# Performance work log

Hardware: AMD Instinct MI355X
Metric: run time of the kernel (lower is better)

Reference implementation:

```python
import jax, jax.numpy as jnp
import numpy as np

N = 20000      # atom nodes
E_UND = 200000 # undirected edges -> E = 2*E_UND directed, stored as interleaved reverse pairs
D = 128        # hid_dim
H = 4          # heads (fixed in MVMP)
DEPTH = 3


def _build_graph():
    rng = np.random.default_rng(0)
    u_chain = np.arange(N - 1)
    v_chain = u_chain + 1
    n_extra = E_UND - (N - 1)
    ue = rng.integers(0, N, n_extra)
    ve = rng.integers(0, N, n_extra)
    ve = np.where(ue == ve, (ve + 1) % N, ve)
    u = np.concatenate([u_chain, ue])
    v = np.concatenate([v_chain, ve])
    # interleave so that edge 2k = u->v and edge 2k+1 = v->u (reverse_edge pairing)
    src = np.stack([u, v], 1).reshape(-1).astype(np.int32)
    dst = np.stack([v, u], 1).reshape(-1).astype(np.int32)
    return jnp.asarray(src), jnp.asarray(dst)


def setup_inputs() -> dict:
    key = jax.random.key(0)
    ks = jax.random.split(key, 10)
    src, dst = _build_graph()
    E = src.shape[0]
    s = 1.0 / np.sqrt(D)

    def lin(k, shape):
        return (jax.random.normal(k, shape, jnp.float32) * s).astype(jnp.float32)

    return {
        "f": jax.random.normal(ks[0], (N, D), jnp.float32),
        "x": jax.random.normal(ks[1], (E, D), jnp.float32),
        "src": src,
        "dst": dst,
        "Wq": lin(ks[2], (D, D)), "bq": jnp.zeros((D,), jnp.float32),
        "Wk": lin(ks[3], (D, D)), "bk": jnp.zeros((D,), jnp.float32),
        "Wv": lin(ks[4], (D, D)), "bv": jnp.zeros((D,), jnp.float32),
        "Wo": lin(ks[5], (D, D)), "bo": jnp.zeros((D,), jnp.float32),
        "W_mp": lin(ks[6], (DEPTH - 1, D, D)),
        "b_mp": jnp.zeros((DEPTH - 1, D), jnp.float32),
        "W_last": lin(ks[7], (3 * D, D)),
        "b_last": jnp.zeros((D,), jnp.float32),
    }


def _mailbox_attention(f_h, h, dst, Wq, bq, Wk, bk, Wv, bv, Wo, bo):
    """add_attn: per-node MHA with query = node state, keys/values = incoming edge msgs.
    Implemented as an edge-segment softmax (no padding), equivalent to DGL degree bucketing."""
    n = f_h.shape[0]
    dk = D // H
    q = (f_h @ Wq + bq).reshape(n, H, dk)     # [N,H,dk]
    k = (h @ Wk + bk).reshape(-1, H, dk)      # [E,H,dk]
    v = (h @ Wv + bv).reshape(-1, H, dk)      # [E,H,dk]
    scores = jnp.einsum("ehd,ehd->eh", q[dst], k) / jnp.sqrt(jnp.float32(dk))  # [E,H]
    smax = jax.ops.segment_max(scores, dst, num_segments=n)   # [N,H]
    p = jnp.exp(scores - smax[dst])
    denom = jax.ops.segment_sum(p, dst, num_segments=n)       # [N,H]
    ctx = jax.ops.segment_sum(p[:, :, None] * v, dst, num_segments=n) / denom[:, :, None]
    out = ctx.reshape(n, D) @ Wo + bo
    return out + f_h  # residual in add_attn


def reference(f, x, src, dst, Wq, bq, Wk, bk, Wv, bv, Wo, bo, W_mp, b_mp, W_last, b_last):
    n, E = f.shape[0], x.shape[0]
    f_h = f          # init_node: f_h = f.clone()
    h = x            # init_edge: h = x.clone()
    for i in range(DEPTH - 1):
        # multi_update_all: copy_e('h','m') then add_attn on node states
        f_h = _mailbox_attention(f_h, h, dst, Wq, bq, Wk, bk, Wv, bv, Wo, bo)
        # rev_h = reverse_edge(h): swap interleaved pairs
        rev_h = h.reshape(E // 2, 2, D)[:, ::-1, :].reshape(E, D)
        # del_reverse_message: m = f_h[src] - rev_h
        m = f_h[src] - rev_h
        # update_edge: h = relu(x + Linear_i(m))
        h = jax.nn.relu(x + m @ W_mp[i] + b_mp[i])
    # final: copy_e('h','mail') then update_node with Linear(3D->D)
    mail = jax.ops.segment_sum(h, dst, num_segments=n)
    return jnp.concatenate([mail, f_h, f], axis=1) @ W_last + b_last
```

## Files before the change

### kernel.cpp

```cpp
#include <hip/hip_runtime.h>
#include <hip/hip_bf16.h>

typedef __attribute__((ext_vector_type(8))) short bf16x8;
typedef __attribute__((ext_vector_type(4))) float f32x4;

__device__ __forceinline__ unsigned short f2bf(float f) {
    unsigned u = __float_as_uint(f);
    unsigned r = (u + 0x7FFFu + ((u >> 16) & 1u)) >> 16;
    return (unsigned short)r;
}
__device__ __forceinline__ float bf2f(unsigned short b) {
    return __uint_as_float(((unsigned)b) << 16);
}
__device__ __forceinline__ unsigned pack2(float a, float b) {
    return (unsigned)f2bf(a) | ((unsigned)f2bf(b) << 16);
}
__device__ __forceinline__ unsigned pksub(unsigned a, unsigned b) {
    float r0 = bf2f((unsigned short)(a & 0xffff)) - bf2f((unsigned short)(b & 0xffff));
    float r1 = bf2f((unsigned short)(a >> 16))    - bf2f((unsigned short)(b >> 16));
    return pack2(r0, r1);
}
#define EXP2(x) __builtin_amdgcn_exp2f(x)

__device__ __forceinline__ void gload_lds16(const void* g, void* l) {
    __builtin_amdgcn_global_load_lds(
        (const __attribute__((address_space(1))) unsigned int*)g,
        (__attribute__((address_space(3))) unsigned int*)l,
        16, 0, 0);
}

template<int RES, bool OUT_BF16, bool OUT2>
__global__ __launch_bounds__(256, 4) void gemm_s(
    const unsigned short* __restrict__ A, const unsigned short* __restrict__ WT,
    const float* __restrict__ bias, const void* res,
    void* out, unsigned short* __restrict__ out2, int M, int ntiles)
{
    __shared__ __align__(16) unsigned short As[2][64 * 128];

    const int t = threadIdx.x, wave = t >> 6, lane = t & 63;
    const int lr = lane & 15, lk = lane >> 4;

    bf16x8 Bf[4][2];
    f32x4 bs[2];
#pragma unroll
    for (int fn = 0; fn < 2; fn++) {
        const int col0 = wave * 32 + fn * 16 + lk * 4;
        bs[fn] = bias ? *reinterpret_cast<const f32x4*>(bias + col0)
                      : (f32x4){0.f, 0.f, 0.f, 0.f};
        const int n = wave * 32 + fn * 16 + lr;
#pragma unroll
        for (int kk = 0; kk < 4; kk++)
            Bf[kk][fn] = *reinterpret_cast<const bf16x8*>(WT + n * 128 + kk * 32 + lk * 8);
    }

    auto stage = [&](int buf, int row0) {
#pragma unroll
        for (int i = 0; i < 4; i++) {
            const int flat = (wave * 4 + i) * 1024 + lane * 16;
            const int r = flat >> 8, c = (flat >> 4) & 15;
            int gr = row0 + r; if (gr >= M) gr = M - 1;
            const void* g = A + (size_t)gr * 128 + ((c ^ (r & 7)) << 3);
            void* l = (void*)((char*)&As[buf][0] + (size_t)(wave * 4 + i) * 1024);
            gload_lds16(g, l);
        }
    };

    int tt = blockIdx.x;
    if (tt >= ntiles) return;
    int cur = 0;
    stage(0, tt * 64);
    __syncthreads();

    for (; tt < ntiles; tt += gridDim.x) {
        const int nxt = tt + gridDim.x;
        if (nxt < ntiles) stage(cur ^ 1, nxt * 64);

        f32x4 acc[4][2];
#pragma unroll
        for (int a = 0; a < 4; a++)
#pragma unroll
            for (int b = 0; b < 2; b++) acc[a][b] = (f32x4){0.f, 0.f, 0.f, 0.f};

#pragma unroll
        for (int kk = 0; kk < 4; kk++) {
            bf16x8 af[4];
#pragma unroll
            for (int fm = 0; fm < 4; fm++) {
                const int r = fm * 16 + lr;
                const int c = (kk * 4 + lk) ^ (r & 7);
                af[fm] = *reinterpret_cast<const bf16x8*>(&As[cur][r * 128 + c * 8]);
            }
#pragma unroll
            for (int fm = 0; fm < 4; fm++)
#pragma unroll
                for (int fn = 0; fn < 2; fn++)
                    acc[fm][fn] = __builtin_amdgcn_mfma_f32_16x16x32_bf16(
                        Bf[kk][fn], af[fm], acc[fm][fn], 0, 0, 0);
        }

        const int row0 = tt * 64;
#pragma unroll
        for (int fm = 0; fm < 4; fm++) {
            const int row = row0 + fm * 16 + lr;
            if (row < M) {
#pragma unroll
                for (int fn = 0; fn < 2; fn++) {
                    const int col0 = wave * 32 + fn * 16 + lk * 4;
                    const size_t off = (size_t)row * 128 + col0;
                    f32x4 vv = acc[fm][fn] + bs[fn];
                    if (RES == 1)
                        vv += *reinterpret_cast<const f32x4*>((const float*)res + off);
                    if (OUT_BF16) {
                        uint2 o; o.x = pack2(vv[0], vv[1]); o.y = pack2(vv[2], vv[3]);
                        *reinterpret_cast<uint2*>((unsigned short*)out + off) = o;
                    } else {
                        *reinterpret_cast<f32x4*>((float*)out + off) = vv;
                    }
                    if (OUT2) {
                        uint2 o; o.x = pack2(vv[0], vv[1]); o.y = pack2(vv[2], vv[3]);
                        *reinterpret_cast<uint2*>(out2 + off) = o;
                    }
                }
            }
        }
        __syncthreads();
        cur ^= 1;
    }
}

__global__ __launch_bounds__(512, 2) void gemm_q512(
    const unsigned short* __restrict__ A, const unsigned short* __restrict__ WT,
    const float* __restrict__ bias, unsigned short* __restrict__ out, int M)
{
    __shared__ __align__(16) unsigned short As[64 * 128];

    const int t = threadIdx.x, wave = t >> 6, lane = t & 63;
    const int lr = lane & 15, lk = lane >> 4;

    bf16x8 Bf[4][4];
    f32x4 bs[4];
#pragma unroll
    for (int fn = 0; fn < 4; fn++) {
        const int col0 = wave * 64 + fn * 16 + lk * 4;
        bs[fn] = *reinterpret_cast<const f32x4*>(bias + col0);
        const int n = wave * 64 + fn * 16 + lr;
#pragma unroll
        for (int kk = 0; kk < 4; kk++)
            Bf[kk][fn] = *reinterpret_cast<const bf16x8*>(WT + n * 128 + kk * 32 + lk * 8);
    }

    const int row0 = blockIdx.x * 64;
#pragma unroll
    for (int i = 0; i < 2; i++) {
        const int flat = (i * 512 + t) * 16;
        const int r = flat >> 8, c = (flat >> 4) & 15;
        int gr = row0 + r; if (gr >= M) gr = M - 1;
        const void* g = A + (size_t)gr * 128 + ((c ^ (r & 7)) << 3);
        void* l = (void*)((char*)&As[0] + (size_t)(i * 512 + wave * 64) * 16 + 0);
        gload_lds16(g, l);
    }
    __syncthreads();

    f32x4 acc[4][4];
#pragma unroll
    for (int a = 0; a < 4; a++)
#pragma unroll
        for (int b = 0; b < 4; b++) acc[a][b] = (f32x4){0.f, 0.f, 0.f, 0.f};

#pragma unroll
    for (int kk = 0; kk < 4; kk++) {
        bf16x8 af[4];
#pragma unroll
        for (int fm = 0; fm < 4; fm++) {
            const int r = fm * 16 + lr;
            const int c = (kk * 4 + lk) ^ (r & 7);
            af[fm] = *reinterpret_cast<const bf16x8*>(&As[r * 128 + c * 8]);
        }
#pragma unroll
        for (int fm = 0; fm < 4; fm++)
#pragma unroll
            for (int fn = 0; fn < 4; fn++)
                acc[fm][fn] = __builtin_amdgcn_mfma_f32_16x16x32_bf16(
                    Bf[kk][fn], af[fm], acc[fm][fn], 0, 0, 0);
    }

#pragma unroll
    for (int fm = 0; fm < 4; fm++) {
        const int row = row0 + fm * 16 + lr;
        if (row < M) {
#pragma unroll
            for (int fn = 0; fn < 4; fn++) {
                const int col0 = wave * 64 + fn * 16 + lk * 4;
                f32x4 vv = acc[fm][fn] + bs[fn];
                uint2 o; o.x = pack2(vv[0], vv[1]); o.y = pack2(vv[2], vv[3]);
                *reinterpret_cast<uint2*>(out + (size_t)row * 512 + col0) = o;
            }
        }
    }
}

__global__ __launch_bounds__(256, 2) void gemm_k512(
    const unsigned short* __restrict__ A, const unsigned short* __restrict__ WT,
    const float* __restrict__ bias, float* __restrict__ f_h,
    unsigned short* __restrict__ f_hb, int M)
{
    __shared__ __align__(16) unsigned short As[64 * 512];

    const int t = threadIdx.x, wave = t >> 6, lane = t & 63;
    const int lr = lane & 15, lk = lane >> 4;

    bf16x8 Bf[16][2];
    f32x4 bs[2];
#pragma unroll
    for (int fn = 0; fn < 2; fn++) {
        const int col0 = wave * 32 + fn * 16 + lk * 4;
        bs[fn] = *reinterpret_cast<const f32x4*>(bias + col0);
        const int n = wave * 32 + fn * 16 + lr;
#pragma unroll
        for (int kk = 0; kk < 16; kk++)
            Bf[kk][fn] = *reinterpret_cast<const bf16x8*>(WT + n * 512 + kk * 32 + lk * 8);
    }

    const int row0 = blockIdx.x * 64;
#pragma unroll
    for (int i = 0; i < 16; i++) {
        const int flat = (i * 256 + t) * 16;
        const int r = flat >> 10, c = (flat >> 4) & 63;
        int gr = row0 + r; if (gr >= M) gr = M - 1;
        const void* g = A + (size_t)gr * 512 + ((c ^ (r & 7)) << 3);
        void* l = (void*)((char*)&As[0] + (size_t)(i * 256 + wave * 64) * 16);
        gload_lds16(g, l);
    }
    __syncthreads();

    f32x4 acc[4][2];
#pragma unroll
    for (int a = 0; a < 4; a++)
#pragma unroll
        for (int b = 0; b < 2; b++) acc[a][b] = (f32x4){0.f, 0.f, 0.f, 0.f};

#pragma unroll
    for (int kk = 0; kk < 16; kk++) {
        bf16x8 af[4];
#pragma unroll
        for (int fm = 0; fm < 4; fm++) {
            const int r = fm * 16 + lr;
            const int c = (kk * 4 + lk) ^ (r & 7);
            af[fm] = *reinterpret_cast<const bf16x8*>(&As[r * 512 + c * 8]);
        }
#pragma unroll
        for (int fm = 0; fm < 4; fm++)
#pragma unroll
            for (int fn = 0; fn < 2; fn++)
                acc[fm][fn] = __builtin_amdgcn_mfma_f32_16x16x32_bf16(
                    Bf[kk][fn], af[fm], acc[fm][fn], 0, 0, 0);
    }

#pragma unroll
    for (int fm = 0; fm < 4; fm++) {
        const int row = row0 + fm * 16 + lr;
        if (row < M) {
#pragma unroll
            for (int fn = 0; fn < 2; fn++) {
                const int col0 = wave * 32 + fn * 16 + lk * 4;
                const size_t off = (size_t)row * 128 + col0;
                f32x4 vv = acc[fm][fn] + bs[fn];
                vv += *reinterpret_cast<const f32x4*>(f_h + off);
                *reinterpret_cast<f32x4*>(f_h + off) = vv;
                uint2 o; o.x = pack2(vv[0], vv[1]); o.y = pack2(vv[2], vv[3]);
                *reinterpret_cast<uint2*>(f_hb + off) = o;
            }
        }
    }
}

__global__ __launch_bounds__(256, 3) void gemm_mrelu(
    const unsigned short* __restrict__ f_hb, const unsigned short* __restrict__ h,
    const int* __restrict__ src, const unsigned short* __restrict__ WT,
    const float* __restrict__ bias, const unsigned short* __restrict__ resx,
    unsigned short* __restrict__ out, int E, int ntiles)
{
    __shared__ __align__(16) unsigned short As[2][64 * 128];

    const int t = threadIdx.x, wave = t >> 6, lane = t & 63;
    const int lr = lane & 15, lk = lane >> 4;

    bf16x8 Bf[4][2];
    f32x4 bs[2];
#pragma unroll
    for (int fn = 0; fn < 2; fn++) {
        const int col0 = wave * 32 + fn * 16 + lk * 4;
        bs[fn] = *reinterpret_cast<const f32x4*>(bias + col0);
        const int n = wave * 32 + fn * 16 + lr;
#pragma unroll
        for (int kk = 0; kk < 4; kk++)
            Bf[kk][fn] = *reinterpret_cast<const bf16x8*>(WT + n * 128 + kk * 32 + lk * 8);
    }

    uint4 Lh[4], Lf[4];
    auto load_t = [&](int row0) {
#pragma unroll
        for (int i = 0; i < 4; i++) {
            const int flat = (wave * 4 + i) * 1024 + lane * 16;
            const int r = flat >> 8, c = (flat >> 4) & 15;
            int e = row0 + r; if (e >= E) e = E - 1;
            Lh[i] = *reinterpret_cast<const uint4*>(h + (size_t)(e ^ 1) * 128 + c * 8);
            const int se = src[e];
            Lf[i] = *reinterpret_cast<const uint4*>(f_hb + (size_t)se * 128 + c * 8);
        }
    };
    auto write_t = [&](int buf) {
#pragma unroll
        for (int i = 0; i < 4; i++) {
            const int flat = (wave * 4 + i) * 1024 + lane * 16;
            const int r = flat >> 8, c = (flat >> 4) & 15;
            uint4 d;
            d.x = pksub(Lf[i].x, Lh[i].x); d.y = pksub(Lf[i].y, Lh[i].y);
            d.z = pksub(Lf[i].z, Lh[i].z); d.w = pksub(Lf[i].w, Lh[i].w);
            *reinterpret_cast<uint4*>(&As[buf][r * 128 + ((c ^ (r & 7)) << 3)]) = d;
        }
    };

    int tt = blockIdx.x;
    if (tt >= ntiles) return;
    load_t(tt * 64);
    write_t(0);
    int cur = 0;
    __syncthreads();

    for (; tt < ntiles; tt += gridDim.x) {
        const int nxt = tt + gridDim.x;
        if (nxt < ntiles) load_t(nxt * 64);

        f32x4 acc[4][2];
#pragma unroll
        for (int a = 0; a < 4; a++)
#pragma unroll
            for (int b = 0; b < 2; b++) acc[a][b] = (f32x4){0.f, 0.f, 0.f, 0.f};

#pragma unroll
        for (int kk = 0; kk < 4; kk++) {
            bf16x8 af[4];
#pragma unroll
            for (int fm = 0; fm < 4; fm++) {
                const int r = fm * 16 + lr;
                const int c = (kk * 4 + lk) ^ (r & 7);
                af[fm] = *reinterpret_cast<const bf16x8*>(&As[cur][r * 128 + c * 8]);
            }
#pragma unroll
            for (int fm = 0; fm < 4; fm++)
#pragma unroll
                for (int fn = 0; fn < 2; fn++)
                    acc[fm][fn] = __builtin_amdgcn_mfma_f32_16x16x32_bf16(
                        Bf[kk][fn], af[fm], acc[fm][fn], 0, 0, 0);
        }

        const int row0 = tt * 64;
#pragma unroll
        for (int fm = 0; fm < 4; fm++) {
            const int row = row0 + fm * 16 + lr;
            if (row < E) {
#pragma unroll
                for (int fn = 0; fn < 2; fn++) {
                    const int col0 = wave * 32 + fn * 16 + lk * 4;
                    const size_t off = (size_t)row * 128 + col0;
                    f32x4 vv = acc[fm][fn] + bs[fn];
                    uint2 rb = *reinterpret_cast<const uint2*>(resx + off);
                    vv[0] += bf2f((unsigned short)(rb.x & 0xffff));
                    vv[1] += bf2f((unsigned short)(rb.x >> 16));
                    vv[2] += bf2f((unsigned short)(rb.y & 0xffff));
                    vv[3] += bf2f((unsigned short)(rb.y >> 16));
                    vv[0] = fmaxf(vv[0], 0.f); vv[1] = fmaxf(vv[1], 0.f);
                    vv[2] = fmaxf(vv[2], 0.f); vv[3] = fmaxf(vv[3], 0.f);
                    uint2 o; o.x = pack2(vv[0], vv[1]); o.y = pack2(vv[2], vv[3]);
                    *reinterpret_cast<uint2*>(out + off) = o;
                }
            }
        }

        if (nxt < ntiles) write_t(cur ^ 1);
        __syncthreads();
        cur ^= 1;
    }
}

__global__ void hist_kernel(const int* __restrict__ dst, int* __restrict__ deg, int E_) {
    int e = blockIdx.x * 256 + threadIdx.x;
    if (e < E_) atomicAdd(&deg[dst[e]], 1);
}

__global__ __launch_bounds__(1024) void scan_kernel(
    const int* __restrict__ deg, int* __restrict__ rowptr,
    int* __restrict__ cursor, int N_)
{
    __shared__ int part[1024];
    const int t = threadIdx.x;
    const int chunk = (N_ + 1023) >> 10;
    const int base = t * chunk;
    int s = 0;
    for (int i = 0; i < chunk; i++) {
        int idx = base + i;
        if (idx < N_) s += deg[idx];
    }
    part[t] = s;
    __syncthreads();
    for (int off = 1; off < 1024; off <<= 1) {
        int v = (t >= off) ? part[t - off] : 0;
        __syncthreads();
        part[t] += v;
        __syncthreads();
    }
    int run = (t == 0) ? 0 : part[t - 1];
    for (int i = 0; i < chunk; i++) {
        int idx = base + i;
        if (idx < N_) {
            rowptr[idx] = run;
            cursor[idx] = run;
            run += deg[idx];
        }
    }
    if (t == 1023) rowptr[N_] = part[1023];
}

__global__ void scatter_kernel(const int* __restrict__ dst, int* __restrict__ cursor,
                               int* __restrict__ eidx, int E_) {
    int e = blockIdx.x * 256 + threadIdx.x;
    if (e >= E_) return;
    int pos = atomicAdd(&cursor[dst[e]], 1);
    eidx[pos] = e;
}

__global__ __launch_bounds__(256) void attn_fused(
    const unsigned short* __restrict__ qkt, const unsigned short* __restrict__ h,
    const int* __restrict__ rowptr, const int* __restrict__ eidx,
    unsigned short* __restrict__ whm, int N_)
{
    const int n = blockIdx.x * 4 + (threadIdx.x >> 6);
    if (n >= N_) return;
    const int lane = threadIdx.x & 63;
    const int g = lane >> 4, s = lane & 15;

    const int beg = rowptr[n], end = rowptr[n + 1];
    unsigned short* outp = whm + (size_t)n * 512 + g * 128 + s * 8;
    if (beg == end) {
        *reinterpret_cast<uint2*>(outp) = make_uint2(0u, 0u);
        *reinterpret_cast<uint2*>(outp + 4) = make_uint2(0u, 0u);
        return;
    }

    float qk[4][8];
#pragma unroll
    for (int hd = 0; hd < 4; hd++) {
        uint4 u = *reinterpret_cast<const uint4*>(qkt + (size_t)n * 512 + hd * 128 + s * 8);
        qk[hd][0] = bf2f((unsigned short)(u.x & 0xffff)); qk[hd][1] = bf2f((unsigned short)(u.x >> 16));
        qk[hd][2] = bf2f((unsigned short)(u.y & 0xffff)); qk[hd][3] = bf2f((unsigned short)(u.y >> 16));
        qk[hd][4] = bf2f((unsigned short)(u.z & 0xffff)); qk[hd][5] = bf2f((unsigned short)(u.z >> 16));
        qk[hd][6] = bf2f((unsigned short)(u.w & 0xffff)); qk[hd][7] = bf2f((unsigned short)(u.w >> 16));
    }

    float m[4], l[4], a[4][8];
#pragma unroll
    for (int hd = 0; hd < 4; hd++) {
        m[hd] = -3.0e38f; l[hd] = 0.f;
#pragma unroll
        for (int j = 0; j < 8; j++) a[hd][j] = 0.f;
    }

    const int T = (end - beg + 3) >> 2;
    int idx = beg + g;
    uint4 hv = make_uint4(0u, 0u, 0u, 0u);
    if (idx < end) hv = *reinterpret_cast<const uint4*>(h + (size_t)eidx[idx] * 128 + s * 8);

    for (int it = 0; it < T; it++) {
        const uint4 hc = hv;
        const bool valid = (idx < end);
        const int nidx = idx + 4;
        if (nidx < end) hv = *reinterpret_cast<const uint4*>(h + (size_t)eidx[nidx] * 128 + s * 8);
        idx = nidx;

        float hf[8];
        hf[0] = bf2f((unsigned short)(hc.x & 0xffff)); hf[1] = bf2f((unsigned short)(hc.x >> 16));
        hf[2] = bf2f((unsigned short)(hc.y & 0xffff)); hf[3] = bf2f((unsigned short)(hc.y >> 16));
        hf[4] = bf2f((unsigned short)(hc.z & 0xffff)); hf[5] = bf2f((unsigned short)(hc.z >> 16));
        hf[6] = bf2f((unsigned short)(hc.w & 0xffff)); hf[7] = bf2f((unsigned short)(hc.w >> 16));

        float part[4];
#pragma unroll
        for (int hd = 0; hd < 4; hd++) {
            float pp = 0.f;
#pragma unroll
            for (int j = 0; j < 8; j++) pp += qk[hd][j] * hf[j];
            part[hd] = pp;
        }
#pragma unroll
        for (int off = 1; off < 16; off <<= 1) {
#pragma unroll
            for (int hd = 0; hd < 4; hd++)
                part[hd] += __shfl_xor(part[hd], off, 64);
        }

        if (valid) {
#pragma unroll
            for (int hd = 0; hd < 4; hd++) {
                const float sv = part[hd];
                const float mn = fmaxf(m[hd], sv);
                const float sc = EXP2(m[hd] - mn);
                const float pp = EXP2(sv - mn);
                l[hd] = l[hd] * sc + pp;
#pragma unroll
                for (int j = 0; j < 8; j++) a[hd][j] = a[hd][j] * sc + pp * hf[j];
                m[hd] = mn;
            }
        }
    }

#pragma unroll
    for (int off = 16; off <= 32; off <<= 1) {
#pragma unroll
        for (int hd = 0; hd < 4; hd++) {
            const float mo = __shfl_xor(m[hd], off, 64);
            const float lo = __shfl_xor(l[hd], off, 64);
            const float mn = fmaxf(m[hd], mo);
            const float sc = EXP2(m[hd] - mn);
            const float so = EXP2(mo - mn);
            l[hd] = l[hd] * sc + lo * so;
#pragma unroll
            for (int j = 0; j < 8; j++) {
                const float ao = __shfl_xor(a[hd][j], off, 64);
                a[hd][j] = a[hd][j] * sc + ao * so;
            }
            m[hd] = mn;
        }
    }

#pragma unroll
    for (int hd = 0; hd < 4; hd++) {
        if (g == hd) {
            const float rl = 1.f / l[hd];
            uint4 o;
            o.x = pack2(a[hd][0] * rl, a[hd][1] * rl);
            o.y = pack2(a[hd][2] * rl, a[hd][3] * rl);
            o.z = pack2(a[hd][4] * rl, a[hd][5] * rl);
            o.w = pack2(a[hd][6] * rl, a[hd][7] * rl);
            *reinterpret_cast<uint4*>(outp) = o;
        }
    }
}

__global__ __launch_bounds__(256) void mail_csr(
    const unsigned short* __restrict__ h,
    const int* __restrict__ rowptr, const int* __restrict__ eidx,
    unsigned short* __restrict__ mailb, int N_)
{
    const int n = blockIdx.x * 4 + (threadIdx.x >> 6);
    if (n >= N_) return;
    const int lane = threadIdx.x & 63;
    const int g = lane >> 4, s = lane & 15;

    const int beg = rowptr[n], end = rowptr[n + 1];

    float a[8];
#pragma unroll
    for (int j = 0; j < 8; j++) a[j] = 0.f;

    const int T = (end - beg + 3) >> 2;
    int idx = beg + g;
    uint4 hv = make_uint4(0u, 0u, 0u, 0u);
    if (idx < end) hv = *reinterpret_cast<const uint4*>(h + (size_t)eidx[idx] * 128 + s * 8);

    for (int it = 0; it < T; it++) {
        const uint4 hc = hv;
        const bool valid = (idx < end);
        const int nidx = idx + 4;
        if (nidx < end) hv = *reinterpret_cast<const uint4*>(h + (size_t)eidx[nidx] * 128 + s * 8);
        idx = nidx;
        if (valid) {
            a[0] += bf2f((unsigned short)(hc.x & 0xffff)); a[1] += bf2f((unsigned short)(hc.x >> 16));
            a[2] += bf2f((unsigned short)(hc.y & 0xffff)); a[3] += bf2f((unsigned short)(hc.y >> 16));
            a[4] += bf2f((unsigned short)(hc.z & 0xffff)); a[5] += bf2f((unsigned short)(hc.z >> 16));
            a[6] += bf2f((unsigned short)(hc.w & 0xffff)); a[7] += bf2f((unsigned short)(hc.w >> 16));
        }
    }
#pragma unroll
    for (int off = 16; off <= 32; off <<= 1)
#pragma unroll
        for (int j = 0; j < 8; j++) a[j] += __shfl_xor(a[j], off, 64);

    if (g == 0) {
        uint4 o;
        o.x = pack2(a[0], a[1]); o.y = pack2(a[2], a[3]);
        o.z = pack2(a[4], a[5]); o.w = pack2(a[6], a[7]);
        *reinterpret_cast<uint4*>(mailb + (size_t)n * 128 + s * 8) = o;
    }
}

struct W5 { const float* p[5]; };

__global__ void cvt_wT(W5 w, unsigned short* __restrict__ out) {
    const float* src = w.p[blockIdx.x];
    unsigned short* dst = out + (size_t)blockIdx.x * 16384;
    for (int idx = threadIdx.x; idx < 16384; idx += 256) {
        const int k = idx >> 7, n = idx & 127;
        dst[n * 128 + k] = f2bf(src[idx]);
    }
}

#define SCORE_SCALE 0.25508994161f

__global__ void mcat_kernel(const float* __restrict__ Wq, const float* __restrict__ Wk,
                            const float* __restrict__ bq,
                            unsigned short* __restrict__ McatT, float* __restrict__ cbias) {
    const int oc = blockIdx.x;
    const int hd = oc >> 7, ip = oc & 127;
    const int a = threadIdx.x;
    const float* wk = Wk + ip * 128 + hd * 32;
    const float* wq = Wq + a * 128 + hd * 32;
    float s = 0.f;
    for (int jj = 0; jj < 32; jj++) s += wq[jj] * wk[jj];
    McatT[(size_t)oc * 128 + a] = f2bf(s * SCORE_SCALE);
    if (a == 0) {
        float c = 0.f;
        for (int jj = 0; jj < 32; jj++) c += bq[hd * 32 + jj] * wk[jj];
        cbias[oc] = c * SCORE_SCALE;
    }
}

__global__ void pcat_kernel(const float* __restrict__ Wv, const float* __restrict__ Wo,
                            unsigned short* __restrict__ PcatT) {
    const int j = blockIdx.x;
    const int k = threadIdx.x;
    const int hd = k >> 7, i = k & 127;
    float s = 0.f;
    for (int cc = 0; cc < 32; cc++)
        s += Wv[i * 128 + hd * 32 + cc] * Wo[(hd * 32 + cc) * 128 + j];
    PcatT[(size_t)j * 512 + k] = f2bf(s);
}

__global__ void bias2_kernel(const float* __restrict__ bv, const float* __restrict__ Wo,
                             const float* __restrict__ bo, float* __restrict__ bias2) {
    const int j = threadIdx.x;
    if (j >= 128) return;
    float s = 0.f;
    for (int c = 0; c < 128; c++) s += bv[c] * Wo[c * 128 + j];
    bias2[j] = s + bo[j];
}

__global__ void cvt_bf16(const float* __restrict__ in, unsigned short* __restrict__ out, long n4) {
    long i = (long)blockIdx.x * 256 + threadIdx.x;
    if (i >= n4) return;
    float4 v = reinterpret_cast<const float4*>(in)[i];
    ushort4 o;
    o.x = f2bf(v.x); o.y = f2bf(v.y); o.z = f2bf(v.z); o.w = f2bf(v.w);
    reinterpret_cast<ushort4*>(out)[i] = o;
}

__global__ void prep_f(const float* __restrict__ f, unsigned short* __restrict__ fb,
                       float* __restrict__ f_h, int n4) {
    int i = blockIdx.x * 256 + threadIdx.x;
    if (i >= n4) return;
    float4 v = reinterpret_cast<const float4*>(f)[i];
    reinterpret_cast<float4*>(f_h)[i] = v;
    ushort4 o;
    o.x = f2bf(v.x); o.y = f2bf(v.y); o.z = f2bf(v.z); o.w = f2bf(v.w);
    reinterpret_cast<ushort4*>(fb)[i] = o;
}

extern "C" void kernel_launch(void* const* d_in, const int* in_sizes, int n_in,
                              void* d_out, int out_size, void* d_ws, size_t ws_size,
                              hipStream_t stream)
{
    const float* f      = (const float*)d_in[0];
    const float* x      = (const float*)d_in[1];
    const int*   src    = (const int*)d_in[2];
    const int*   dst    = (const int*)d_in[3];
    const float* Wq     = (const float*)d_in[4];
    const float* bq     = (const float*)d_in[5];
    const float* Wk     = (const float*)d_in[6];
    const float* bk     = (const float*)d_in[7];
    const float* Wv     = (const float*)d_in[8];
    const float* bv     = (const float*)d_in[9];
    const float* Wo     = (const float*)d_in[10];
    const float* bo     = (const float*)d_in[11];
    const float* W_mp   = (const float*)d_in[12];
    const float* b_mp   = (const float*)d_in[13];
    const float* W_last = (const float*)d_in[14];
    const float* b_last = (const float*)d_in[15];
    (void)bk;

    const int N = in_sizes[0] / 128;
    const int E = in_sizes[1] / 128;

    char* p = (char*)d_ws;
    auto take = [&](size_t bytes) { char* r = p; p += (bytes + 255) & ~(size_t)255; return r; };
    unsigned short* w5T   = (unsigned short*)take(5 * 16384 * 2);
    unsigned short* McatT = (unsigned short*)take(512 * 128 * 2);
    unsigned short* PcatT = (unsigned short*)take(128 * 512 * 2);
    float* cbias  = (float*)take(512 * 4);
    float* bias2  = (float*)take(128 * 4);
    unsigned short* xb    = (unsigned short*)take((size_t)E * 128 * 2);
    unsigned short* h1    = (unsigned short*)take((size_t)E * 128 * 2);
    unsigned short* h2    = (unsigned short*)take((size_t)E * 128 * 2);
    unsigned short* fb    = (unsigned short*)take((size_t)N * 128 * 2);
    unsigned short* f_hb  = (unsigned short*)take((size_t)N * 128 * 2);
    unsigned short* qkt   = (unsigned short*)take((size_t)N * 512 * 2);
    unsigned short* whm   = (unsigned short*)take((size_t)N * 512 * 2);
    unsigned short* mailb = (unsigned short*)take((size_t)N * 128 * 2);
    float* f_h    = (float*)take((size_t)N * 128 * 4);
    int* deg      = (int*)take((size_t)N * 4);
    int* rowptr   = (int*)take((size_t)(N + 1) * 4);
    int* cursor   = (int*)take((size_t)N * 4);
    int* eidx     = (int*)take((size_t)E * 4);

    const unsigned short* Wm0T = w5T + 0 * 16384;
    const unsigned short* Wm1T = w5T + 1 * 16384;
    const unsigned short* WL0T = w5T + 2 * 16384;
    const unsigned short* WL1T = w5T + 3 * 16384;
    const unsigned short* WL2T = w5T + 4 * 16384;

    W5 w5;
    w5.p[0] = W_mp; w5.p[1] = W_mp + 16384;
    w5.p[2] = W_last; w5.p[3] = W_last + 16384; w5.p[4] = W_last + 32768;

    cvt_wT<<<5, 256, 0, stream>>>(w5, w5T);
    mcat_kernel<<<512, 128, 0, stream>>>(Wq, Wk, bq, McatT, cbias);
    pcat_kernel<<<128, 512, 0, stream>>>(Wv, Wo, PcatT);
    bias2_kernel<<<1, 128, 0, stream>>>(bv, Wo, bo, bias2);
    cvt_bf16<<<(int)(((long)E * 32 + 255) / 256), 256, 0, stream>>>(x, xb, (long)E * 32);
    prep_f<<<(N * 32 + 255) / 256, 256, 0, stream>>>(f, fb, f_h, N * 32);

    hipMemsetAsync(deg, 0, (size_t)N * 4, stream);
    hist_kernel<<<(E + 255) / 256, 256, 0, stream>>>(dst, deg, E);
    scan_kernel<<<1, 1024, 0, stream>>>(deg, rowptr, cursor, N);
    scatter_kernel<<<(E + 255) / 256, 256, 0, stream>>>(dst, cursor, eidx, E);

    const int ntN = (N + 63) / 64;
    const int ntE = (E + 63) / 64;
    const int gNode = (N + 3) / 4;

    const unsigned short* hc = xb;
    unsigned short* houts[2] = { h1, h2 };
    for (int it = 0; it < 2; it++) {
        const unsigned short* fh_in = (it == 0) ? fb : f_hb;
        gemm_q512<<<ntN, 512, 0, stream>>>(fh_in, McatT, cbias, qkt, N);
        attn_fused<<<gNode, 256, 0, stream>>>(qkt, hc, rowptr, eidx, whm, N);
        gemm_k512<<<ntN, 256, 0, stream>>>(whm, PcatT, bias2, f_h, f_hb, N);
        gemm_mrelu<<<768, 256, 0, stream>>>(
            f_hb, hc, src, (it == 0) ? Wm0T : Wm1T, b_mp + (size_t)it * 128,
            xb, houts[it], E, ntE);
        hc = houts[it];
    }

    mail_csr<<<gNode, 256, 0, stream>>>(hc, rowptr, eidx, mailb, N);

    gemm_s<0, false, false><<<ntN, 256, 0, stream>>>(
        mailb, WL0T, b_last, nullptr, (float*)d_out, nullptr, N, ntN);
    gemm_s<1, false, false><<<ntN, 256, 0, stream>>>(
        f_hb, WL1T, nullptr, d_out, (float*)d_out, nullptr, N, ntN);
    gemm_s<1, false, false><<<ntN, 256, 0, stream>>>(
        fb, WL2T, nullptr, d_out, (float*)d_out, nullptr, N, ntN);
}
```

Measured before the change: 555.4 us.

## Store edge features in dst-sorted order to remove indirect gathers; fuse final GEMMs

The scatter step now records each edge's position in the dst-sorted CSR order instead of the edge index. The x conversion and the edge-update GEMM also write a permuted copy of their bf16 output in that order. Attention and mail aggregation can then read contiguous rows without going through eidx. The three final 128x128 GEMMs with read-modify-write of the fp32 output are replaced by one kernel that accumulates all three products. In exchange there are extra scattered writes of permuted edge tensors and more registers in the final kernel.

```diff
diff --git a/kernel.cpp b/kernel.cpp
--- a/kernel.cpp
+++ b/kernel.cpp
@@ -27,105 +27,6 @@
         (const __attribute__((address_space(1))) unsigned int*)g,
         (__attribute__((address_space(3))) unsigned int*)l,
         16, 0, 0);
-}
-
-template<int RES, bool OUT_BF16, bool OUT2>
-__global__ __launch_bounds__(256, 4) void gemm_s(
-    const unsigned short* __restrict__ A, const unsigned short* __restrict__ WT,
-    const float* __restrict__ bias, const void* res,
-    void* out, unsigned short* __restrict__ out2, int M, int ntiles)
-{
-    __shared__ __align__(16) unsigned short As[2][64 * 128];
-
-    const int t = threadIdx.x, wave = t >> 6, lane = t & 63;
-    const int lr = lane & 15, lk = lane >> 4;
-
-    bf16x8 Bf[4][2];
-    f32x4 bs[2];
-#pragma unroll
-    for (int fn = 0; fn < 2; fn++) {
-        const int col0 = wave * 32 + fn * 16 + lk * 4;
-        bs[fn] = bias ? *reinterpret_cast<const f32x4*>(bias + col0)
-                      : (f32x4){0.f, 0.f, 0.f, 0.f};
-        const int n = wave * 32 + fn * 16 + lr;
-#pragma unroll
-        for (int kk = 0; kk < 4; kk++)
-            Bf[kk][fn] = *reinterpret_cast<const bf16x8*>(WT + n * 128 + kk * 32 + lk * 8);
-    }
-
-    auto stage = [&](int buf, int row0) {
-#pragma unroll
-        for (int i = 0; i < 4; i++) {
-            const int flat = (wave * 4 + i) * 1024 + lane * 16;
-            const int r = flat >> 8, c = (flat >> 4) & 15;
-            int gr = row0 + r; if (gr >= M) gr = M - 1;
-            const void* g = A + (size_t)gr * 128 + ((c ^ (r & 7)) << 3);
-            void* l = (void*)((char*)&As[buf][0] + (size_t)(wave * 4 + i) * 1024);
-            gload_lds16(g, l);
-        }
-    };
-
-    int tt = blockIdx.x;
-    if (tt >= ntiles) return;
-    int cur = 0;
-    stage(0, tt * 64);
-    __syncthreads();
-
-    for (; tt < ntiles; tt += gridDim.x) {
-        const int nxt = tt + gridDim.x;
-        if (nxt < ntiles) stage(cur ^ 1, nxt * 64);
-
-        f32x4 acc[4][2];
-#pragma unroll
-        for (int a = 0; a < 4; a++)
-#pragma unroll
-            for (int b = 0; b < 2; b++) acc[a][b] = (f32x4){0.f, 0.f, 0.f, 0.f};
-
-#pragma unroll
-        for (int kk = 0; kk < 4; kk++) {
-            bf16x8 af[4];
-#pragma unroll
-            for (int fm = 0; fm < 4; fm++) {
-                const int r = fm * 16 + lr;
-                const int c = (kk * 4 + lk) ^ (r & 7);
-                af[fm] = *reinterpret_cast<const bf16x8*>(&As[cur][r * 128 + c * 8]);
-            }
-#pragma unroll
-            for (int fm = 0; fm < 4; fm++)
-#pragma unroll
-                for (int fn = 0; fn < 2; fn++)
-                    acc[fm][fn] = __builtin_amdgcn_mfma_f32_16x16x32_bf16(
-                        Bf[kk][fn], af[fm], acc[fm][fn], 0, 0, 0);
-        }
-
-        const int row0 = tt * 64;
-#pragma unroll
-        for (int fm = 0; fm < 4; fm++) {
-            const int row = row0 + fm * 16 + lr;
-            if (row < M) {
-#pragma unroll
-                for (int fn = 0; fn < 2; fn++) {
-                    const int col0 = wave * 32 + fn * 16 + lk * 4;
-                    const size_t off = (size_t)row * 128 + col0;
-                    f32x4 vv = acc[fm][fn] + bs[fn];
-                    if (RES == 1)
-                        vv += *reinterpret_cast<const f32x4*>((const float*)res + off);
-                    if (OUT_BF16) {
-                        uint2 o; o.x = pack2(vv[0], vv[1]); o.y = pack2(vv[2], vv[3]);
-                        *reinterpret_cast<uint2*>((unsigned short*)out + off) = o;
-                    } else {
-                        *reinterpret_cast<f32x4*>((float*)out + off) = vv;
-                    }
-                    if (OUT2) {
-                        uint2 o; o.x = pack2(vv[0], vv[1]); o.y = pack2(vv[2], vv[3]);
-                        *reinterpret_cast<uint2*>(out2 + off) = o;
-                    }
-                }
-            }
-        }
-        __syncthreads();
-        cur ^= 1;
-    }
 }
 
 __global__ __launch_bounds__(512, 2) void gemm_q512(
@@ -274,11 +175,14 @@
     }
 }
 
+template<bool WRITE_EDGE>
 __global__ __launch_bounds__(256, 3) void gemm_mrelu(
     const unsigned short* __restrict__ f_hb, const unsigned short* __restrict__ h,
-    const int* __restrict__ src, const unsigned short* __restrict__ WT,
+    const int* __restrict__ src, const int* __restrict__ inv,
+    const unsigned short* __restrict__ WT,
     const float* __restrict__ bias, const unsigned short* __restrict__ resx,
-    unsigned short* __restrict__ out, int E, int ntiles)
+    unsigned short* __restrict__ out, unsigned short* __restrict__ outp,
+    int E, int ntiles)
 {
     __shared__ __align__(16) unsigned short As[2][64 * 128];
 
@@ -360,6 +264,7 @@
         for (int fm = 0; fm < 4; fm++) {
             const int row = row0 + fm * 16 + lr;
             if (row < E) {
+                const int pr = inv[row];
 #pragma unroll
                 for (int fn = 0; fn < 2; fn++) {
                     const int col0 = wave * 32 + fn * 16 + lk * 4;
@@ -373,7 +278,9 @@
                     vv[0] = fmaxf(vv[0], 0.f); vv[1] = fmaxf(vv[1], 0.f);
                     vv[2] = fmaxf(vv[2], 0.f); vv[3] = fmaxf(vv[3], 0.f);
                     uint2 o; o.x = pack2(vv[0], vv[1]); o.y = pack2(vv[2], vv[3]);
-                    *reinterpret_cast<uint2*>(out + off) = o;
+                    if (WRITE_EDGE)
+                        *reinterpret_cast<uint2*>(out + off) = o;
+                    *reinterpret_cast<uint2*>(outp + (size_t)pr * 128 + col0) = o;
                 }
             }
         }
@@ -381,6 +288,91 @@
         if (nxt < ntiles) write_t(cur ^ 1);
         __syncthreads();
         cur ^= 1;
+    }
+}
+
+__global__ __launch_bounds__(256, 2) void gemm_final(
+    const unsigned short* __restrict__ A0, const unsigned short* __restrict__ A1,
+    const unsigned short* __restrict__ A2,
+    const unsigned short* __restrict__ W0T, const unsigned short* __restrict__ W1T,
+    const unsigned short* __restrict__ W2T,
+    const float* __restrict__ bias, float* __restrict__ out, int M)
+{
+    __shared__ __align__(16) unsigned short As[3][64 * 128];
+
+    const int t = threadIdx.x, wave = t >> 6, lane = t & 63;
+    const int lr = lane & 15, lk = lane >> 4;
+
+    const unsigned short* Asrc[3] = { A0, A1, A2 };
+    const unsigned short* Wsrc[3] = { W0T, W1T, W2T };
+
+    bf16x8 Bf[12][2];
+    f32x4 bs[2];
+#pragma unroll
+    for (int fn = 0; fn < 2; fn++) {
+        const int col0 = wave * 32 + fn * 16 + lk * 4;
+        bs[fn] = *reinterpret_cast<const f32x4*>(bias + col0);
+        const int n = wave * 32 + fn * 16 + lr;
+#pragma unroll
+        for (int b = 0; b < 3; b++)
+#pragma unroll
+            for (int kk = 0; kk < 4; kk++)
+                Bf[b * 4 + kk][fn] = *reinterpret_cast<const bf16x8*>(
+                    Wsrc[b] + n * 128 + kk * 32 + lk * 8);
+    }
+
+    const int row0 = blockIdx.x * 64;
+#pragma unroll
+    for (int b = 0; b < 3; b++) {
+#pragma unroll
+        for (int i = 0; i < 4; i++) {
+            const int flat = (wave * 4 + i) * 1024 + lane * 16;
+            const int r = flat >> 8, c = (flat >> 4) & 15;
+            int gr = row0 + r; if (gr >= M) gr = M - 1;
+            const void* g = Asrc[b] + (size_t)gr * 128 + ((c ^ (r & 7)) << 3);
+            void* l = (void*)((char*)&As[b][0] + (size_t)(wave * 4 + i) * 1024);
+            gload_lds16(g, l);
+        }
+    }
+    __syncthreads();
+
+    f32x4 acc[4][2];
+#pragma unroll
+    for (int a = 0; a < 4; a++)
+#pragma unroll
+        for (int b = 0; b < 2; b++) acc[a][b] = (f32x4){0.f, 0.f, 0.f, 0.f};
+
+#pragma unroll
+    for (int b = 0; b < 3; b++) {
+#pragma unroll
+        for (int kk = 0; kk < 4; kk++) {
+            bf16x8 af[4];
+#pragma unroll
+            for (int fm = 0; fm < 4; fm++) {
+                const int r = fm * 16 + lr;
+                const int c = (kk * 4 + lk) ^ (r & 7);
+                af[fm] = *reinterpret_cast<const bf16x8*>(&As[b][r * 128 + c * 8]);
+            }
+#pragma unroll
+            for (int fm = 0; fm < 4; fm++)
+#pragma unroll
+                for (int fn = 0; fn < 2; fn++)
+                    acc[fm][fn] = __builtin_amdgcn_mfma_f32_16x16x32_bf16(
+                        Bf[b * 4 + kk][fn], af[fm], acc[fm][fn], 0, 0, 0);
+        }
+    }
+
+#pragma unroll
+    for (int fm = 0; fm < 4; fm++) {
+        const int row = row0 + fm * 16 + lr;
+        if (row < M) {
+#pragma unroll
+            for (int fn = 0; fn < 2; fn++) {
+                const int col0 = wave * 32 + fn * 16 + lk * 4;
+                *reinterpret_cast<f32x4*>(out + (size_t)row * 128 + col0) =
+                    acc[fm][fn] + bs[fn];
+            }
+        }
     }
 }
 
@@ -423,17 +415,16 @@
 }
 
 __global__ void scatter_kernel(const int* __restrict__ dst, int* __restrict__ cursor,
-                               int* __restrict__ eidx, int E_) {
+                               int* __restrict__ inv, int E_) {
     int e = blockIdx.x * 256 + threadIdx.x;
     if (e >= E_) return;
     int pos = atomicAdd(&cursor[dst[e]], 1);
-    eidx[pos] = e;
+    inv[e] = pos;
 }
 
 __global__ __launch_bounds__(256) void attn_fused(
-    const unsigned short* __restrict__ qkt, const unsigned short* __restrict__ h,
-    const int* __restrict__ rowptr, const int* __restrict__ eidx,
-    unsigned short* __restrict__ whm, int N_)
+    const unsigned short* __restrict__ qkt, const unsigned short* __restrict__ hp,
+    const int* __restrict__ rowptr, unsigned short* __restrict__ whm, int N_)
 {
     const int n = blockIdx.x * 4 + (threadIdx.x >> 6);
     if (n >= N_) return;
@@ -467,16 +458,16 @@
     }
 
     const int T = (end - beg + 3) >> 2;
-    int idx = beg + g;
+    int p = beg + g;
     uint4 hv = make_uint4(0u, 0u, 0u, 0u);
-    if (idx < end) hv = *reinterpret_cast<const uint4*>(h + (size_t)eidx[idx] * 128 + s * 8);
+    if (p < end) hv = *reinterpret_cast<const uint4*>(hp + (size_t)p * 128 + s * 8);
 
     for (int it = 0; it < T; it++) {
         const uint4 hc = hv;
-        const bool valid = (idx < end);
-        const int nidx = idx + 4;
-        if (nidx < end) hv = *reinterpret_cast<const uint4*>(h + (size_t)eidx[nidx] * 128 + s * 8);
-        idx = nidx;
+        const bool valid = (p < end);
+        const int np = p + 4;
+        if (np < end) hv = *reinterpret_cast<const uint4*>(hp + (size_t)np * 128 + s * 8);
+        p = np;
 
         float hf[8];
         hf[0] = bf2f((unsigned short)(hc.x & 0xffff)); hf[1] = bf2f((unsigned short)(hc.x >> 16));
@@ -548,9 +539,8 @@
 }
 
 __global__ __launch_bounds__(256) void mail_csr(
-    const unsigned short* __restrict__ h,
-    const int* __restrict__ rowptr, const int* __restrict__ eidx,
-    unsigned short* __restrict__ mailb, int N_)
+    const unsigned short* __restrict__ hp,
+    const int* __restrict__ rowptr, unsigned short* __restrict__ mailb, int N_)
 {
     const int n = blockIdx.x * 4 + (threadIdx.x >> 6);
     if (n >= N_) return;
@@ -564,16 +554,16 @@
     for (int j = 0; j < 8; j++) a[j] = 0.f;
 
     const int T = (end - beg + 3) >> 2;
-    int idx = beg + g;
+    int p = beg + g;
     uint4 hv = make_uint4(0u, 0u, 0u, 0u);
-    if (idx < end) hv = *reinterpret_cast<const uint4*>(h + (size_t)eidx[idx] * 128 + s * 8);
+    if (p < end) hv = *reinterpret_cast<const uint4*>(hp + (size_t)p * 128 + s * 8);
 
     for (int it = 0; it < T; it++) {
         const uint4 hc = hv;
-        const bool valid = (idx < end);
-        const int nidx = idx + 4;
-        if (nidx < end) hv = *reinterpret_cast<const uint4*>(h + (size_t)eidx[nidx] * 128 + s * 8);
-        idx = nidx;
+        const bool valid = (p < end);
+        const int np = p + 4;
+        if (np < end) hv = *reinterpret_cast<const uint4*>(hp + (size_t)np * 128 + s * 8);
+        p = np;
         if (valid) {
             a[0] += bf2f((unsigned short)(hc.x & 0xffff)); a[1] += bf2f((unsigned short)(hc.x >> 16));
             a[2] += bf2f((unsigned short)(hc.y & 0xffff)); a[3] += bf2f((unsigned short)(hc.y >> 16));
@@ -645,13 +635,20 @@
     bias2[j] = s + bo[j];
 }
 
-__global__ void cvt_bf16(const float* __restrict__ in, unsigned short* __restrict__ out, long n4) {
+__global__ void cvt_x(const float* __restrict__ x, const int* __restrict__ inv,
+                      unsigned short* __restrict__ xb, unsigned short* __restrict__ xp,
+                      long nchunks) {
     long i = (long)blockIdx.x * 256 + threadIdx.x;
-    if (i >= n4) return;
-    float4 v = reinterpret_cast<const float4*>(in)[i];
-    ushort4 o;
-    o.x = f2bf(v.x); o.y = f2bf(v.y); o.z = f2bf(v.z); o.w = f2bf(v.w);
-    reinterpret_cast<ushort4*>(out)[i] = o;
+    if (i >= nchunks) return;
+    const long e = i >> 4;
+    const int c = (int)(i & 15);
+    const float4 v0 = reinterpret_cast<const float4*>(x)[i * 2];
+    const float4 v1 = reinterpret_cast<const float4*>(x)[i * 2 + 1];
+    uint4 o;
+    o.x = pack2(v0.x, v0.y); o.y = pack2(v0.z, v0.w);
+    o.z = pack2(v1.x, v1.y); o.w = pack2(v1.z, v1.w);
+    reinterpret_cast<uint4*>(xb)[i] = o;
+    reinterpret_cast<uint4*>(xp)[(size_t)inv[e] * 16 + c] = o;
 }
 
 __global__ void prep_f(const float* __restrict__ f, unsigned short* __restrict__ fb,
@@ -698,8 +695,9 @@
     float* cbias  = (float*)take(512 * 4);
     float* bias2  = (float*)take(128 * 4);
     unsigned short* xb    = (unsigned short*)take((size_t)E * 128 * 2);
+    unsigned short* xp    = (unsigned short*)take((size_t)E * 128 * 2);
     unsigned short* h1    = (unsigned short*)take((size_t)E * 128 * 2);
-    unsigned short* h2    = (unsigned short*)take((size_t)E * 128 * 2);
+    unsigned short* h1p   = (unsigned short*)take((size_t)E * 128 * 2);
     unsigned short* fb    = (unsigned short*)take((size_t)N * 128 * 2);
     unsigned short* f_hb  = (unsigned short*)take((size_t)N * 128 * 2);
     unsigned short* qkt   = (unsigned short*)take((size_t)N * 512 * 2);
@@ -709,7 +707,7 @@
     int* deg      = (int*)take((size_t)N * 4);
     int* rowptr   = (int*)take((size_t)(N + 1) * 4);
     int* cursor   = (int*)take((size_t)N * 4);
-    int* eidx     = (int*)take((size_t)E * 4);
+    int* inv      = (int*)take((size_t)E * 4);
 
     const unsigned short* Wm0T = w5T + 0 * 16384;
     const unsigned short* Wm1T = w5T + 1 * 16384;
@@ -721,41 +719,36 @@
     w5.p[0] = W_mp; w5.p[1] = W_mp + 16384;
     w5.p[2] = W_last; w5.p[3] = W_last + 16384; w5.p[4] = W_last + 32768;
 
+    hipMemsetAsync(deg, 0, (size_t)N * 4, stream);
+    hist_kernel<<<(E + 255) / 256, 256, 0, stream>>>(dst, deg, E);
+    scan_kernel<<<1, 1024, 0, stream>>>(deg, rowptr, cursor, N);
+    scatter_kernel<<<(E + 255) / 256, 256, 0, stream>>>(dst, cursor, inv, E);
+
     cvt_wT<<<5, 256, 0, stream>>>(w5, w5T);
     mcat_kernel<<<512, 128, 0, stream>>>(Wq, Wk, bq, McatT, cbias);
     pcat_kernel<<<128, 512, 0, stream>>>(Wv, Wo, PcatT);
     bias2_kernel<<<1, 128, 0, stream>>>(bv, Wo, bo, bias2);
-    cvt_bf16<<<(int)(((long)E * 32 + 255) / 256), 256, 0, stream>>>(x, xb, (long)E * 32);
+    cvt_x<<<(int)(((long)E * 16 + 255) / 256), 256, 0, stream>>>(x, inv, xb, xp, (long)E * 16);
     prep_f<<<(N * 32 + 255) / 256, 256, 0, stream>>>(f, fb, f_h, N * 32);
-
-    hipMemsetAsync(deg, 0, (size_t)N * 4, stream);
-    hist_kernel<<<(E + 255) / 256, 256, 0, stream>>>(dst, deg, E);
-    scan_kernel<<<1, 1024, 0, stream>>>(deg, rowptr, cursor, N);
-    scatter_kernel<<<(E + 255) / 256, 256, 0, stream>>>(dst, cursor, eidx, E);
 
     const int ntN = (N + 63) / 64;
     const int ntE = (E + 63) / 64;
     const int gNode = (N + 3) / 4;
 
-    const unsigned short* hc = xb;
-    unsigned short* houts[2] = { h1, h2 };
-    for (int it = 0; it < 2; it++) {
-        const unsigned short* fh_in = (it == 0) ? fb : f_hb;
-        gemm_q512<<<ntN, 512, 0, stream>>>(fh_in, McatT, cbias, qkt, N);
-        attn_fused<<<gNode, 256, 0, stream>>>(qkt, hc, rowptr, eidx, whm, N);
-        gemm_k512<<<ntN, 256, 0, stream>>>(whm, PcatT, bias2, f_h, f_hb, N);
-        gemm_mrelu<<<768, 256, 0, stream>>>(
-            f_hb, hc, src, (it == 0) ? Wm0T : Wm1T, b_mp + (size_t)it * 128,
-            xb, houts[it], E, ntE);
-        hc = houts[it];
-    }
-
-    mail_csr<<<gNode, 256, 0, stream>>>(hc, rowptr, eidx, mailb, N);
-
-    gemm_s<0, false, false><<<ntN, 256, 0, stream>>>(
-        mailb, WL0T, b_last, nullptr, (float*)d_out, nullptr, N, ntN);
-    gemm_s<1, false, false><<<ntN, 256, 0, stream>>>(
-        f_hb, WL1T, nullptr, d_out, (float*)d_out, nullptr, N, ntN);
-    gemm_s<1, false, false><<<ntN, 256, 0, stream>>>(
-        fb, WL2T, nullptr, d_out, (float*)d_out, nullptr, N, ntN);
-}
+    gemm_q512<<<ntN, 512, 0, stream>>>(fb, McatT, cbias, qkt, N);
+    attn_fused<<<gNode, 256, 0, stream>>>(qkt, xp, rowptr, whm, N);
+    gemm_k512<<<ntN, 256, 0, stream>>>(whm, PcatT, bias2, f_h, f_hb, N);
+    gemm_mrelu<true><<<768, 256, 0, stream>>>(
+        f_hb, xb, src, inv, Wm0T, b_mp, xb, h1, h1p, E, ntE);
+
+    gemm_q512<<<ntN, 512, 0, stream>>>(f_hb, McatT, cbias, qkt, N);
+    attn_fused<<<gNode, 256, 0, stream>>>(qkt, h1p, rowptr, whm, N);
+    gemm_k512<<<ntN, 256, 0, stream>>>(whm, PcatT, bias2, f_h, f_hb, N);
+    gemm_mrelu<false><<<768, 256, 0, stream>>>(
+        f_hb, h1, src, inv, Wm1T, b_mp + 128, xb, nullptr, xp, E, ntE);
+
+    mail_csr<<<gNode, 256, 0, stream>>>(xp, rowptr, mailb, N);
+
+    gemm_final<<<ntN, 256, 0, stream>>>(
+        mailb, f_hb, fb, WL0T, WL1T, WL2T, b_last, (float*)d_out, N);
+}
```

New measurement: 606.8 us. +9.2%, slower.
